# Optimization experiments

Measured on AMD Instinct MI355X. Metric: run time of the kernel, lower is better.

The kernel has to match this reference:

```python
import jax, jax.numpy as jnp
import numpy as np

EPS = 1e-8  # torch F.cosine_similarity clamps norms at eps=1e-8


def setup_inputs() -> dict:
    key = jax.random.key(0)
    N, M, D = 1024, 20, 768  # speakers, utterances/speaker, embed dim
    embeddings = jax.random.normal(key, (N, M, D), dtype=jnp.float32)
    w = jnp.asarray(10.0, dtype=jnp.float32)  # init_w
    b = jnp.asarray(-5.0, dtype=jnp.float32)  # init_b
    return {"embeddings": embeddings, "w": w, "b": b}


def reference(embeddings, w, b):
    N, M, D = embeddings.shape
    centroids = embeddings.mean(axis=1)  # [N, D]
    # cosine similarity as one fused GEMM on normalized vectors
    e = embeddings / jnp.maximum(
        jnp.linalg.norm(embeddings, axis=-1, keepdims=True), EPS)
    c = centroids / jnp.maximum(
        jnp.linalg.norm(centroids, axis=-1, keepdims=True), EPS)
    # sim[j, i, m] = cos(e[i, m], centroid[j])  -- matches the torch loop/stack
    sim = jnp.einsum('imd,jd->jim', e, c)
    logits = w * sim + b  # [N_j, N_i, M]
    # torch: view(N*N, M).transpose(0,1).reshape(-1, N)
    #   => row index r = m*N + j, column i
    logits = jnp.transpose(logits, (2, 0, 1)).reshape(N * M, N)
    # torch labels: arange(N) expanded over M -> labels[r] = r // M
    labels = jnp.repeat(jnp.arange(N), M)
    logp = jax.nn.log_softmax(logits, axis=-1)
    loss = -jnp.mean(logp[jnp.arange(N * M), labels])
    return loss
```

## Files before the change

### kernel.cpp

```cpp
#include <hip/hip_runtime.h>
#include <hip/hip_bf16.h>
#include <cstdint>

#define N_SPK 1024
#define M_UTT 20
#define D_DIM 768
#define NM_ROWS (N_SPK * M_UTT)

static constexpr float EPS = 1e-8f;

typedef __attribute__((ext_vector_type(4))) float floatx4;
typedef __attribute__((ext_vector_type(2))) long longx2;

__device__ __forceinline__ void load16_to_lds(const void* g, void* l) {
    __builtin_amdgcn_global_load_lds(
        (const __attribute__((address_space(1))) uint32_t*)g,
        (__attribute__((address_space(3))) uint32_t*)l, 16, 0, 0);
}

__device__ __forceinline__ float wave_sum(float v) {
    #pragma unroll
    for (int o = 32; o > 0; o >>= 1) v += __shfl_xor(v, o);
    return v;
}

__device__ __forceinline__ unsigned short fp8pk(float a, float b) {
    return (unsigned short)(__builtin_amdgcn_cvt_pk_fp8_f32(a, b, 0, false) & 0xFFFF);
}

__device__ __forceinline__ int kperm(int d) {
    return (d & ~63) | (((d >> 3) & 3) << 4) | (((d >> 5) & 1) << 3) | (d & 7);
}

__global__ __launch_bounds__(384) void prep_kernel(const float* __restrict__ emb,
                                                   unsigned char* __restrict__ ehat,
                                                   unsigned char* __restrict__ chat,
                                                   int* __restrict__ ctr,
                                                   float* __restrict__ accum) {
    const int i = blockIdx.x;
    const int t = threadIdx.x;
    const int wave = t >> 6, lane = t & 63;

    if (i == 0 && t == 0) { *ctr = 0; *accum = 0.f; }

    const float2* src = (const float2*)(emb + (size_t)i * M_UTT * D_DIM);
    const int dp = kperm(t * 2);

    float2 v[M_UTT];
    float ss[M_UTT];
    float2 cen = {0.f, 0.f};
    #pragma unroll
    for (int m = 0; m < M_UTT; ++m) {
        const float2 x = src[m * 384 + t];
        v[m] = x;
        ss[m] = x.x * x.x + x.y * x.y;
        cen.x += x.x; cen.y += x.y;
    }
    cen.x *= (1.f / M_UTT); cen.y *= (1.f / M_UTT);
    float css = cen.x * cen.x + cen.y * cen.y;

    __shared__ float red[M_UTT + 1][6];
    #pragma unroll
    for (int m = 0; m < M_UTT; ++m) {
        const float s = wave_sum(ss[m]);
        if (lane == 0) red[m][wave] = s;
    }
    {
        const float s = wave_sum(css);
        if (lane == 0) red[M_UTT][wave] = s;
    }
    __syncthreads();

    #pragma unroll
    for (int m = 0; m < M_UTT; ++m) {
        const float tot = red[m][0] + red[m][1] + red[m][2] +
                          red[m][3] + red[m][4] + red[m][5];
        const float rn = 1.0f / fmaxf(sqrtf(tot), EPS);
        *(unsigned short*)(ehat + ((size_t)(m * N_SPK + i)) * D_DIM + dp) =
            fp8pk(v[m].x * rn, v[m].y * rn);
    }
    {
        const float tot = red[M_UTT][0] + red[M_UTT][1] + red[M_UTT][2] +
                          red[M_UTT][3] + red[M_UTT][4] + red[M_UTT][5];
        const float rn = 1.0f / fmaxf(sqrtf(tot), EPS);
        *(unsigned short*)(chat + (size_t)i * D_DIM + dp) =
            fp8pk(cen.x * rn, cen.y * rn);
    }
}

__global__ __launch_bounds__(256, 4) void gemm_fused_kernel(
        const unsigned char* __restrict__ ehat,
        const unsigned char* __restrict__ chat,
        const float* __restrict__ wp,
        float* __restrict__ Psum,
        float* __restrict__ T) {
    __shared__ unsigned char As[2][128 * 64];
    __shared__ unsigned char Bs[2][128 * 64];

    const int t    = threadIdx.x;
    const int lane = t & 63;
    const int wid  = t >> 6;
    const int c    = lane & 15;
    const int quad = lane >> 4;
    const int wr   = wid >> 1;
    const int wc   = wid & 1;

    const int xcd = blockIdx.x & 7;
    const int idx = blockIdx.x >> 3;
    const int bu  = xcd * 20 + (idx >> 3);
    const int bj  = idx & 7;
    const int m   = bu >> 3;
    const int rb8 = bu & 7;
    const int u0  = bu * 128;
    const int j0  = bj * 128;

    const unsigned char* Ag = ehat + (size_t)u0 * D_DIM;
    const unsigned char* Bg = chat + (size_t)j0 * D_DIM;

    int goff[2];
    #pragma unroll
    for (int s = 0; s < 2; ++s) {
        const int ci  = s * 256 + wid * 64 + lane;
        const int row = ci >> 2;
        const int qg  = (ci & 3) ^ ((row >> 1) & 3);
        goff[s] = row * D_DIM + qg * 16;
    }

    int slotA[4], slotB[4];
    #pragma unroll
    for (int f = 0; f < 4; ++f) {
        const int rA = wr * 64 + f * 16 + c;
        const int rB = wc * 64 + f * 16 + c;
        slotA[f] = rA * 64 + ((quad ^ ((rA >> 1) & 3)) * 16);
        slotB[f] = rB * 64 + ((quad ^ ((rB >> 1) & 3)) * 16);
    }

    floatx4 acc[4][4] = {};

    #pragma unroll
    for (int s = 0; s < 2; ++s) {
        load16_to_lds(Ag + goff[s], &As[0][(s * 256 + wid * 64 + lane) * 16]);
        load16_to_lds(Bg + goff[s], &Bs[0][(s * 256 + wid * 64 + lane) * 16]);
    }
    __syncthreads();

    #pragma unroll
    for (int kt = 0; kt < 12; ++kt) {
        const int cur = kt & 1;
        const int nxt = cur ^ 1;

        if (kt < 11) {
            const int k0 = (kt + 1) * 64;
            #pragma unroll
            for (int s = 0; s < 2; ++s) {
                load16_to_lds(Ag + goff[s] + k0,
                              &As[nxt][(s * 256 + wid * 64 + lane) * 16]);
                load16_to_lds(Bg + goff[s] + k0,
                              &Bs[nxt][(s * 256 + wid * 64 + lane) * 16]);
            }
        }

        longx2 af[4], bf[4];
        #pragma unroll
        for (int f = 0; f < 4; ++f)
            af[f] = *(const longx2*)(&As[cur][slotA[f]]);
        #pragma unroll
        for (int f = 0; f < 4; ++f)
            bf[f] = *(const longx2*)(&Bs[cur][slotB[f]]);

        #pragma unroll
        for (int ks = 0; ks < 2; ++ks)
            #pragma unroll
            for (int it = 0; it < 4; ++it)
                #pragma unroll
                for (int jt = 0; jt < 4; ++jt)
                    acc[it][jt] = __builtin_amdgcn_mfma_f32_16x16x32_fp8_fp8(
                        af[it][ks], bf[jt][ks], acc[it][jt], 0, 0, 0);

        if (kt < 11) __syncthreads();
    }

    const float w = wp[0];
    const int rb320 = bu * 2 + wr;

    #pragma unroll
    for (int jt = 0; jt < 4; ++jt) {
        float sm = 0.f;
        #pragma unroll
        for (int it = 0; it < 4; ++it)
            #pragma unroll
            for (int r = 0; r < 4; ++r)
                sm += __expf(w * (acc[it][jt][r] - 1.0f));
        sm += __shfl_xor(sm, 16);
        sm += __shfl_xor(sm, 32);
        if (quad == 0)
            Psum[(size_t)rb320 * N_SPK + j0 + wc * 64 + jt * 16 + c] = sm;
    }

    #pragma unroll
    for (int it = 0; it < 4; ++it) {
        #pragma unroll
        for (int jt = 0; jt < 4; ++jt) {
            const int col = j0 + wc * 64 + jt * 16 + c;
            const int g = m * N_SPK + col;
            const int istar = g / M_UTT;
            const int rloc = rb8 * 128 + wr * 64 + it * 16 + quad * 4;
            #pragma unroll
            for (int r = 0; r < 4; ++r) {
                if (rloc + r == istar) T[g] = acc[it][jt][r];
            }
        }
    }
}

__global__ void combine_kernel(const float* __restrict__ Psum,
                               const float* __restrict__ T,
                               const float* __restrict__ wp,
                               int* __restrict__ ctr,
                               float* __restrict__ accum,
                               float* __restrict__ out) {
    const int p = blockIdx.x * 256 + threadIdx.x;
    const int m = p >> 10;
    const int j = p & 1023;
    const float w = wp[0];

    float S = 0.f;
    #pragma unroll
    for (int rb = 0; rb < 16; ++rb)
        S += Psum[(size_t)(m * 16 + rb) * N_SPK + j];
    const float term = w * (T[p] - 1.0f) - __logf(S);

    __shared__ float red[256];
    red[threadIdx.x] = term;
    __syncthreads();
    for (int o = 128; o > 0; o >>= 1) {
        if (threadIdx.x < o) red[threadIdx.x] += red[threadIdx.x + o];
        __syncthreads();
    }
    if (threadIdx.x == 0) {
        atomicAdd(accum, red[0]);
        __threadfence();
        const int old = atomicAdd(ctr, 1);
        if (old == 79) {
            const float a = atomicAdd(accum, 0.0f);
            out[0] = -a / (float)NM_ROWS;
        }
    }
}

extern "C" void kernel_launch(void* const* d_in, const int* in_sizes, int n_in,
                              void* d_out, int out_size, void* d_ws, size_t ws_size,
                              hipStream_t stream) {
    const float* emb = (const float*)d_in[0];
    const float* wp  = (const float*)d_in[1];
    float* out = (float*)d_out;

    char* ws = (char*)d_ws;
    unsigned char* ehat = (unsigned char*)(ws);
    unsigned char* chat = (unsigned char*)(ws + 15728640);
    float* Psum  = (float*)(ws + 16515072);
    float* T     = (float*)(ws + 17825792);
    int*   ctr   = (int*)  (ws + 17907712);
    float* accum = (float*)(ws + 17907716);

    prep_kernel<<<dim3(N_SPK), dim3(384), 0, stream>>>(emb, ehat, chat, ctr, accum);
    gemm_fused_kernel<<<dim3(1280), dim3(256), 0, stream>>>(ehat, chat, wp, Psum, T);
    combine_kernel<<<dim3(80), dim3(256), 0, stream>>>(Psum, T, wp, ctr, accum, out);
}
```

Baseline: 131.7 us.

## Use gfx950 scaled 16x16x128 fp8 MFMA with 128-wide K tiles

Replaces the 16x16x32 fp8 MFMA with the MI355X scaled 16x16x128 f8f6f4 MFMA using unit scales, and doubles the K tile to 128 so there are half as many K iterations and barriers. LDS tiles, swizzle and global-to-LDS load mapping are redone for 128-byte rows, and launch bounds drop to 2 blocks per CU to fit the larger LDS footprint. This cuts MFMA issue count and synchronization, at the cost of lower occupancy and more LDS per block. Correctness depends on the operand layout of the new MFMA matching the permuted K ordering used by the prep kernel.

```diff
diff --git a/kernel.cpp b/kernel.cpp
--- a/kernel.cpp
+++ b/kernel.cpp
@@ -10,7 +10,8 @@
 static constexpr float EPS = 1e-8f;
 
 typedef __attribute__((ext_vector_type(4))) float floatx4;
-typedef __attribute__((ext_vector_type(2))) long longx2;
+typedef __attribute__((ext_vector_type(4))) int   intx4;
+typedef __attribute__((ext_vector_type(8))) int   intx8;
 
 __device__ __forceinline__ void load16_to_lds(const void* g, void* l) {
     __builtin_amdgcn_global_load_lds(
@@ -88,14 +89,14 @@
     }
 }
 
-__global__ __launch_bounds__(256, 4) void gemm_fused_kernel(
+__global__ __launch_bounds__(256, 2) void gemm_fused_kernel(
         const unsigned char* __restrict__ ehat,
         const unsigned char* __restrict__ chat,
         const float* __restrict__ wp,
         float* __restrict__ Psum,
         float* __restrict__ T) {
-    __shared__ unsigned char As[2][128 * 64];
-    __shared__ unsigned char Bs[2][128 * 64];
+    __shared__ unsigned char As[2][128 * 128];
+    __shared__ unsigned char Bs[2][128 * 128];
 
     const int t    = threadIdx.x;
     const int lane = t & 63;
@@ -117,13 +118,13 @@
     const unsigned char* Ag = ehat + (size_t)u0 * D_DIM;
     const unsigned char* Bg = chat + (size_t)j0 * D_DIM;
 
-    int goff[2];
-    #pragma unroll
-    for (int s = 0; s < 2; ++s) {
-        const int ci  = s * 256 + wid * 64 + lane;
-        const int row = ci >> 2;
-        const int qg  = (ci & 3) ^ ((row >> 1) & 3);
-        goff[s] = row * D_DIM + qg * 16;
+    int goff[4];
+    #pragma unroll
+    for (int s = 0; s < 4; ++s) {
+        const int ci  = s * 256 + t;
+        const int row = ci >> 3;
+        const int l   = (ci & 7) ^ (row & 7);
+        goff[s] = row * D_DIM + l * 16;
     }
 
     int slotA[4], slotB[4];
@@ -131,53 +132,58 @@
     for (int f = 0; f < 4; ++f) {
         const int rA = wr * 64 + f * 16 + c;
         const int rB = wc * 64 + f * 16 + c;
-        slotA[f] = rA * 64 + ((quad ^ ((rA >> 1) & 3)) * 16);
-        slotB[f] = rB * 64 + ((quad ^ ((rB >> 1) & 3)) * 16);
+        slotA[f] = rA * 128 + ((quad ^ (c & 7)) * 16);
+        slotB[f] = rB * 128 + ((quad ^ (c & 7)) * 16);
     }
 
     floatx4 acc[4][4] = {};
 
     #pragma unroll
-    for (int s = 0; s < 2; ++s) {
-        load16_to_lds(Ag + goff[s], &As[0][(s * 256 + wid * 64 + lane) * 16]);
-        load16_to_lds(Bg + goff[s], &Bs[0][(s * 256 + wid * 64 + lane) * 16]);
+    for (int s = 0; s < 4; ++s) {
+        load16_to_lds(Ag + goff[s], &As[0][(s * 256 + t) * 16]);
+        load16_to_lds(Bg + goff[s], &Bs[0][(s * 256 + t) * 16]);
     }
     __syncthreads();
 
     #pragma unroll
-    for (int kt = 0; kt < 12; ++kt) {
+    for (int kt = 0; kt < 6; ++kt) {
         const int cur = kt & 1;
         const int nxt = cur ^ 1;
 
-        if (kt < 11) {
-            const int k0 = (kt + 1) * 64;
-            #pragma unroll
-            for (int s = 0; s < 2; ++s) {
-                load16_to_lds(Ag + goff[s] + k0,
-                              &As[nxt][(s * 256 + wid * 64 + lane) * 16]);
-                load16_to_lds(Bg + goff[s] + k0,
-                              &Bs[nxt][(s * 256 + wid * 64 + lane) * 16]);
+        if (kt < 5) {
+            const int k0 = (kt + 1) * 128;
+            #pragma unroll
+            for (int s = 0; s < 4; ++s) {
+                load16_to_lds(Ag + goff[s] + k0, &As[nxt][(s * 256 + t) * 16]);
+                load16_to_lds(Bg + goff[s] + k0, &Bs[nxt][(s * 256 + t) * 16]);
             }
         }
 
-        longx2 af[4], bf[4];
-        #pragma unroll
-        for (int f = 0; f < 4; ++f)
-            af[f] = *(const longx2*)(&As[cur][slotA[f]]);
-        #pragma unroll
-        for (int f = 0; f < 4; ++f)
-            bf[f] = *(const longx2*)(&Bs[cur][slotB[f]]);
-
-        #pragma unroll
-        for (int ks = 0; ks < 2; ++ks)
-            #pragma unroll
-            for (int it = 0; it < 4; ++it)
-                #pragma unroll
-                for (int jt = 0; jt < 4; ++jt)
-                    acc[it][jt] = __builtin_amdgcn_mfma_f32_16x16x32_fp8_fp8(
-                        af[it][ks], bf[jt][ks], acc[it][jt], 0, 0, 0);
-
-        if (kt < 11) __syncthreads();
+        intx8 av[4], bv[4];
+        #pragma unroll
+        for (int f = 0; f < 4; ++f) {
+            const intx4 lo = *(const intx4*)(&As[cur][slotA[f]]);
+            const intx4 hi = *(const intx4*)(&As[cur][slotA[f] ^ 64]);
+            av[f] = __builtin_shufflevector(lo, hi, 0, 1, 2, 3, 4, 5, 6, 7);
+        }
+        #pragma unroll
+        for (int f = 0; f < 4; ++f) {
+            const intx4 lo = *(const intx4*)(&Bs[cur][slotB[f]]);
+            const intx4 hi = *(const intx4*)(&Bs[cur][slotB[f] ^ 64]);
+            bv[f] = __builtin_shufflevector(lo, hi, 0, 1, 2, 3, 4, 5, 6, 7);
+        }
+
+        #pragma unroll
+        for (int it = 0; it < 4; ++it)
+            #pragma unroll
+            for (int jt = 0; jt < 4; ++jt)
+                acc[it][jt] = __builtin_amdgcn_mfma_scale_f32_16x16x128_f8f6f4(
+                    av[it], bv[jt], acc[it][jt],
+                    0, 0,
+                    0, 0x7F7F7F7F,
+                    0, 0x7F7F7F7F);
+
+        if (kt < 5) __syncthreads();
     }
 
     const float w = wp[0];
```

Result: no change. 129.9 us, median of 2 (-1.4%).
